# Kernel optimization log

Measured on AMD Instinct MI355X. Metric: run time of the kernel, lower is better.

Reference implementation:

```python
import jax, jax.numpy as jnp
import numpy as np

B, T, EMB_D, HEAD = 8, 2048, 1024, 128


def setup_inputs() -> dict:
    key = jax.random.key(0)
    ks = jax.random.split(key, 7)
    s = 1.0 / np.sqrt(EMB_D)
    return {
        "inputs": jax.random.normal(ks[0], (B, T, EMB_D), dtype=jnp.float32),
        "Wk": jax.random.uniform(ks[1], (EMB_D, HEAD), jnp.float32, -s, s),
        "bk": jax.random.uniform(ks[2], (HEAD,), jnp.float32, -s, s),
        "Wq": jax.random.uniform(ks[3], (EMB_D, HEAD), jnp.float32, -s, s),
        "bq": jax.random.uniform(ks[4], (HEAD,), jnp.float32, -s, s),
        "Wv": jax.random.uniform(ks[5], (EMB_D, HEAD), jnp.float32, -s, s),
        "bv": jax.random.uniform(ks[6], (HEAD,), jnp.float32, -s, s),
    }


def reference(inputs, Wk, bk, Wq, bq, Wv, bv):
    # inputs: [B, T, C]
    Bq, Tq, _ = inputs.shape
    k = inputs @ Wk + bk  # [B, T, H]
    q = inputs @ Wq + bq
    v = inputs @ Wv + bv
    scale = HEAD ** -0.5
    weights = jnp.einsum("bth,bsh->bts", q, k) * scale  # [B, T, T]
    causal = jnp.tril(jnp.ones((Tq, Tq), dtype=bool))
    weights = jnp.where(causal, weights, -jnp.inf)
    # NOTE: original code applies softmax over dim=1 (the query axis), faithfully reproduced
    weights = jax.nn.softmax(weights, axis=1)
    return jnp.einsum("bts,bsh->bth", weights, v)  # [B, T, H]
```

## Files before the change

kernel.cpp:

```cpp
#include <hip/hip_runtime.h>
#include <hip/hip_bf16.h>

#define T_SEQ 2048
#define NBATCH 8
#define EMB 1024
#define HD 128

typedef _Float16 f16_t;
typedef _Float16 f16x8 __attribute__((ext_vector_type(8)));
typedef _Float16 f16x4 __attribute__((ext_vector_type(4)));
typedef float f32x4 __attribute__((ext_vector_type(4)));


__device__ __forceinline__ void g2l(const f16_t* g, f16_t* l) {
    __builtin_amdgcn_global_load_lds(
        (const __attribute__((address_space(1))) unsigned int*)g,
        (__attribute__((address_space(3))) unsigned int*)l, 16, 0, 0);
}

__global__ __launch_bounds__(256) void prep(
    const float* __restrict__ Wk, const float* __restrict__ bk,
    const float* __restrict__ Wq, const float* __restrict__ bq,
    const float* __restrict__ Wv, const float* __restrict__ bv,
    f16_t* __restrict__ w2, float* __restrict__ biasc) {
    int n = blockIdx.x;
    int t = threadIdx.x;
    const float scale = 0.08838834764831845f;
    const float* W; const float* bias; float sc; int col;
    if (n < 128)      { W = Wq; bias = bq; sc = scale; col = n; }
    else if (n < 256) { W = Wk; bias = bk; sc = 1.0f;  col = n - 128; }
    else              { W = Wv; bias = bv; sc = 1.0f;  col = n - 256; }
    if (t < 128) {
        int k0 = t * 8;
        f16x8 v;
        #pragma unroll
        for (int i = 0; i < 8; ++i) v[i] = (f16_t)(W[(size_t)(k0 + i) * HD + col] * sc);
        *(f16x8*)&w2[(size_t)(n >> 4) * 16384 + (size_t)(k0 >> 3) * 128 + (n & 15) * 8] = v;
    }
    if (t == 0) biasc[n] = bias[col] * sc;
}

__global__ __launch_bounds__(256) void qkv_gemm(
    const float* __restrict__ X, const f16_t* __restrict__ w2,
    const float* __restrict__ biasc,
    f16_t* __restrict__ q2, f16_t* __restrict__ k2, f16_t* __restrict__ v2) {
    __shared__ f16_t Xs[2][64 * 72];
    __shared__ __align__(16) f16_t Bl[2][8 * 1024];

    int bid = blockIdx.x;
    int r8 = bid & 7, g = bid >> 3;
    int band = (g / 3) * 8 + r8;
    int i = g % 3;
    int m0 = band * 64, n0 = i * 128;
    int tid = threadIdx.x;
    int lane = tid & 63, w = tid >> 6;
    int quad = lane >> 4, l15 = lane & 15;
    int msub = (w & 1) * 32, nsub = (w >> 1) * 64;

    int srow = tid >> 2;
    int scg  = (tid & 3) * 16;

    const float* xrow = X + (size_t)(m0 + srow) * EMB + scg;
    const f16_t* bbase = w2 + (size_t)(n0 >> 4) * 16384;

    f32x4 acc[2][4] = {};
    float4 pf[4];

    auto loadA = [&](int kc) {
        #pragma unroll
        for (int u = 0; u < 4; ++u) pf[u] = *(const float4*)(xrow + kc * 64 + u * 4);
    };
    auto stageB = [&](int kc, int buf) {
        const f16_t* bsrc = bbase + (size_t)kc * 1024;
        #pragma unroll
        for (int ii = 0; ii < 4; ++ii) {
            int D = tid * 16 + ii * 4096;
            g2l(bsrc + (size_t)(D >> 11) * 16384 + ((D & 2047) >> 1),
                &Bl[buf][D >> 1]);
        }
    };
    auto stageA = [&](int buf) {
        union { f16_t h[8]; uint4 u4; } p0, p1;
        p0.h[0] = (f16_t)pf[0].x; p0.h[1] = (f16_t)pf[0].y;
        p0.h[2] = (f16_t)pf[0].z; p0.h[3] = (f16_t)pf[0].w;
        p0.h[4] = (f16_t)pf[1].x; p0.h[5] = (f16_t)pf[1].y;
        p0.h[6] = (f16_t)pf[1].z; p0.h[7] = (f16_t)pf[1].w;
        p1.h[0] = (f16_t)pf[2].x; p1.h[1] = (f16_t)pf[2].y;
        p1.h[2] = (f16_t)pf[2].z; p1.h[3] = (f16_t)pf[2].w;
        p1.h[4] = (f16_t)pf[3].x; p1.h[5] = (f16_t)pf[3].y;
        p1.h[6] = (f16_t)pf[3].z; p1.h[7] = (f16_t)pf[3].w;
        *(uint4*)&Xs[buf][srow * 72 + scg] = p0.u4;
        *(uint4*)&Xs[buf][srow * 72 + scg + 8] = p1.u4;
    };
    auto compute = [&](int buf) {
        #pragma unroll
        for (int ks = 0; ks < 2; ++ks) {
            f16x8 afr0 = *(const f16x8*)&Xs[buf][(msub + l15) * 72 + ks * 32 + quad * 8];
            f16x8 afr1 = *(const f16x8*)&Xs[buf][(msub + 16 + l15) * 72 + ks * 32 + quad * 8];
            #pragma unroll
            for (int nf = 0; nf < 4; ++nf) {
                int ntl = (nsub >> 4) + nf;
                f16x8 bfr = *(const f16x8*)&Bl[buf][ntl * 1024 + (ks * 4 + quad) * 128 + l15 * 8];
                acc[0][nf] = __builtin_amdgcn_mfma_f32_16x16x32_f16(afr0, bfr, acc[0][nf], 0, 0, 0);
                acc[1][nf] = __builtin_amdgcn_mfma_f32_16x16x32_f16(afr1, bfr, acc[1][nf], 0, 0, 0);
            }
        }
    };

    loadA(0);
    stageB(0, 0);
    stageA(0);
    __syncthreads();

    for (int kc = 0; kc < 16; ++kc) {
        int cur = kc & 1, nxt = cur ^ 1;
        if (kc + 1 < 16) {
            loadA(kc + 1);
            stageB(kc + 1, nxt);
        }
        compute(cur);
        if (kc + 1 < 16) stageA(nxt);
        __syncthreads();
    }

    #pragma unroll
    for (int nf = 0; nf < 4; ++nf) {
        int ng = n0 + nsub + nf * 16 + l15;
        float bval = biasc[ng];
        #pragma unroll
        for (int mf = 0; mf < 2; ++mf) {
            int rowg = m0 + msub + mf * 16 + quad * 4;
            f32x4 a = acc[mf][nf];
            if (ng < 256) {
                f16_t* dst = (ng < 128) ? q2 : k2;
                int c = ng & 127;
                #pragma unroll
                for (int r = 0; r < 4; ++r) {
                    int row = rowg + r;
                    dst[(size_t)(row >> 4) * 2048 + (c >> 3) * 128 + (row & 15) * 8 + (c & 7)]
                        = (f16_t)(a[r] + bval);
                }
            } else {
                int h = ng - 256;
                f16x4 hv;
                #pragma unroll
                for (int r = 0; r < 4; ++r) hv[r] = (f16_t)(a[r] + bval);
                *(f16x4*)&v2[(size_t)(rowg >> 3) * 1024 + h * 8 + (rowg & 7)] = hv;
            }
        }
    }
}

__global__ __launch_bounds__(256, 4) void col_stats(
    const f16_t* __restrict__ q2, const f16_t* __restrict__ k2,
    float* __restrict__ colsum) {
    int bid = blockIdx.x;
    int b = bid & 7;
    int item = 143 - (bid >> 3);
    int cg = 0, slab = 0, cum = 0;
    for (int c = 0; c < 32; ++c) {
        int n = (32 - c + 3) >> 2;
        if (item < cum + n) { cg = c; slab = item - cum; break; }
        cum += n;
    }
    int tc0 = cg + slab * 4, tc1 = min(tc0 + 4, 32);

    int tid = threadIdx.x, lane = tid & 63, w = tid >> 6;
    int quad = lane >> 4, l15 = lane & 15;
    int brow = b * 128;
    size_t base = (size_t)b * T_SEQ;

    f16x8 bfrs[4][4];
    #pragma unroll
    for (int st = 0; st < 4; ++st) {
        const f16_t* kt = k2 + (size_t)(brow + cg * 4 + st) * 2048 + l15 * 8;
        #pragma unroll
        for (int kf = 0; kf < 4; ++kf)
            bfrs[st][kf] = *(const f16x8*)(kt + (kf * 4 + quad) * 128);
    }

    float lacc[4] = {0.f, 0.f, 0.f, 0.f};

    for (int tc = tc0; tc < tc1; ++tc) {
        int tb = tc * 64;
        f16x8 afr[4];
        const f16_t* qt = q2 + (size_t)(brow + tc * 4 + w) * 2048 + l15 * 8;
        #pragma unroll
        for (int kf = 0; kf < 4; ++kf)
            afr[kf] = *(const f16x8*)(qt + (kf * 4 + quad) * 128);
        #pragma unroll
        for (int st = 0; st < 4; ++st) {
            f32x4 s = {};
            #pragma unroll
            for (int kf = 0; kf < 4; ++kf)
                s = __builtin_amdgcn_mfma_f32_16x16x32_f16(afr[kf], bfrs[st][kf], s, 0, 0, 0);
            int scol = cg * 64 + st * 16 + l15;
            #pragma unroll
            for (int r = 0; r < 4; ++r) {
                int t = tb + w * 16 + quad * 4 + r;
                if (t >= scol) lacc[st] += __expf(s[r]);
            }
        }
    }

    #pragma unroll
    for (int st = 0; st < 4; ++st) {
        float v = lacc[st];
        v += __shfl_xor(v, 16, 64);
        v += __shfl_xor(v, 32, 64);
        if (quad == 0) atomicAdd(&colsum[base + cg * 64 + st * 16 + l15], v);
    }
}

__global__ __launch_bounds__(256, 4) void attn_out(
    const f16_t* __restrict__ q2, const f16_t* __restrict__ k2,
    const f16_t* __restrict__ v2, const float* __restrict__ colsum,
    float* __restrict__ out) {
    __shared__ __align__(16) f16_t Kl[4 * 2048];
    __shared__ __align__(16) f16_t Vl[8 * 1024];
    __shared__ __align__(16) f16_t Pl[32 * 72];

    int bid = blockIdx.x;
    int b = bid & 7;
    int item = 159 - (bid >> 3);
    int g = 0, slab = 0, cum = 0;
    for (int gg = 0; gg < 64; ++gg) {
        int n = (((gg >> 1) + 1) + 7) >> 3;
        if (item < cum + n) { g = gg; slab = item - cum; break; }
        cum += n;
    }
    int nch = (g >> 1) + 1;
    int c0 = slab * 8, c1 = min(c0 + 8, nch);
    int trow = g * 32;

    int tid = threadIdx.x, lane = tid & 63, w = tid >> 6;
    int quad = lane >> 4, l15 = lane & 15;
    int brow = b * 128;
    size_t base = (size_t)b * T_SEQ;

    f16x8 qfr[2][4];
    #pragma unroll
    for (int tt = 0; tt < 2; ++tt) {
        const f16_t* qt = q2 + (size_t)(brow + 2 * g + tt) * 2048 + l15 * 8;
        #pragma unroll
        for (int kf = 0; kf < 4; ++kf)
            qfr[tt][kf] = *(const f16x8*)(qt + (kf * 4 + quad) * 128);
    }

    f32x4 o[2][2] = {};

    for (int c = c0; c < c1; ++c) {
        int sb = c * 64;
        __syncthreads();
        const f16_t* ksrc = k2 + (size_t)(brow + (sb >> 4)) * 2048;
        const f16_t* vsrc = v2 + (((size_t)base + sb) >> 3) * 1024;
        #pragma unroll
        for (int i = 0; i < 4; ++i) {
            g2l(ksrc + i * 2048 + tid * 8, Kl + i * 2048 + tid * 8);
            g2l(vsrc + i * 2048 + tid * 8, Vl + i * 2048 + tid * 8);
        }
        __syncthreads();

        float iv = 1.0f / colsum[base + sb + w * 16 + l15];
        int scol = sb + w * 16 + l15;
        f16x8 bfr[4];
        #pragma unroll
        for (int kf = 0; kf < 4; ++kf)
            bfr[kf] = *(const f16x8*)&Kl[w * 2048 + (kf * 4 + quad) * 128 + l15 * 8];
        #pragma unroll
        for (int tt = 0; tt < 2; ++tt) {
            f32x4 s = {};
            #pragma unroll
            for (int kf = 0; kf < 4; ++kf)
                s = __builtin_amdgcn_mfma_f32_16x16x32_f16(qfr[tt][kf], bfr[kf], s, 0, 0, 0);
            #pragma unroll
            for (int r = 0; r < 4; ++r) {
                int t = trow + tt * 16 + quad * 4 + r;
                float pv = (t >= scol) ? __expf(s[r]) * iv : 0.f;
                Pl[(tt * 16 + quad * 4 + r) * 72 + w * 16 + l15] = (f16_t)pv;
            }
        }
        __syncthreads();

        #pragma unroll
        for (int kf2 = 0; kf2 < 2; ++kf2) {
            f16x8 pa0 = *(const f16x8*)&Pl[(l15) * 72 + kf2 * 32 + quad * 8];
            f16x8 pa1 = *(const f16x8*)&Pl[(16 + l15) * 72 + kf2 * 32 + quad * 8];
            #pragma unroll
            for (int hh = 0; hh < 2; ++hh) {
                f16x8 vfr = *(const f16x8*)&Vl[(kf2 * 4 + quad) * 1024 + (w * 32 + hh * 16 + l15) * 8];
                o[0][hh] = __builtin_amdgcn_mfma_f32_16x16x32_f16(pa0, vfr, o[0][hh], 0, 0, 0);
                o[1][hh] = __builtin_amdgcn_mfma_f32_16x16x32_f16(pa1, vfr, o[1][hh], 0, 0, 0);
            }
        }
    }

    #pragma unroll
    for (int tt = 0; tt < 2; ++tt)
        #pragma unroll
        for (int hh = 0; hh < 2; ++hh)
            #pragma unroll
            for (int r = 0; r < 4; ++r)
                atomicAdd(&out[(base + trow + tt * 16 + quad * 4 + r) * HD + w * 32 + hh * 16 + l15],
                          o[tt][hh][r]);
}

extern "C" void kernel_launch(void* const* d_in, const int* in_sizes, int n_in,
                              void* d_out, int out_size, void* d_ws, size_t ws_size,
                              hipStream_t stream) {
    const float* X  = (const float*)d_in[0];
    const float* Wk = (const float*)d_in[1];
    const float* bk = (const float*)d_in[2];
    const float* Wq = (const float*)d_in[3];
    const float* bq = (const float*)d_in[4];
    const float* Wv = (const float*)d_in[5];
    const float* bv = (const float*)d_in[6];
    float* out = (float*)d_out;

    char* ws = (char*)d_ws;
    const size_t W2_B    = 24 * 16384 * 2;
    const size_t BIAS_B  = 2048;
    const size_t QKV_B   = (size_t)NBATCH * T_SEQ * HD * 2;
    f16_t* w2     = (f16_t*)ws;
    float* biasc  = (float*)(ws + W2_B);
    f16_t* q2     = (f16_t*)(ws + W2_B + BIAS_B);
    f16_t* k2     = (f16_t*)(ws + W2_B + BIAS_B + QKV_B);
    f16_t* v2     = (f16_t*)(ws + W2_B + BIAS_B + 2 * QKV_B);
    float* colsum = (float*)(ws + W2_B + BIAS_B + 3 * QKV_B);

    hipMemsetAsync(out, 0, (size_t)NBATCH * T_SEQ * HD * sizeof(float), stream);
    hipMemsetAsync(colsum, 0, (size_t)NBATCH * T_SEQ * sizeof(float), stream);

    prep<<<dim3(384), dim3(256), 0, stream>>>(Wk, bk, Wq, bq, Wv, bv, w2, biasc);
    qkv_gemm<<<dim3(768), dim3(256), 0, stream>>>(X, w2, biasc, q2, k2, v2);
    col_stats<<<dim3(1152), dim3(256), 0, stream>>>(q2, k2, colsum);
    attn_out<<<dim3(1280), dim3(256), 0, stream>>>(q2, k2, v2, colsum, out);
}
```

Measured before the change: 177.6 us.

## Load K/V fragments straight to registers with double-buffered prefetch in attn_out

Drops the shared-memory staging of K and V in attn_out. Each wave now loads its MFMA fragments directly from global memory into registers, prefetching the next chunk while the current one computes, and P is double-buffered in LDS so only one barrier is needed per chunk. This removes LDS traffic and two barriers per chunk, in exchange for higher register pressure (launch bounds lowered from 4 to 3 blocks) and uncoalesced-ish direct global fragment loads.

```diff
diff --git a/kernel.cpp b/kernel.cpp
--- a/kernel.cpp
+++ b/kernel.cpp
@@ -212,13 +212,11 @@
     }
 }
 
-__global__ __launch_bounds__(256, 4) void attn_out(
+__global__ __launch_bounds__(256, 3) void attn_out(
     const f16_t* __restrict__ q2, const f16_t* __restrict__ k2,
     const f16_t* __restrict__ v2, const float* __restrict__ colsum,
     float* __restrict__ out) {
-    __shared__ __align__(16) f16_t Kl[4 * 2048];
-    __shared__ __align__(16) f16_t Vl[8 * 1024];
-    __shared__ __align__(16) f16_t Pl[32 * 72];
+    __shared__ __align__(16) f16_t Pl[2][32 * 72];
 
     int bid = blockIdx.x;
     int b = bid & 7;
@@ -249,50 +247,70 @@
 
     f32x4 o[2][2] = {};
 
-    for (int c = c0; c < c1; ++c) {
-        int sb = c * 64;
-        __syncthreads();
-        const f16_t* ksrc = k2 + (size_t)(brow + (sb >> 4)) * 2048;
-        const f16_t* vsrc = v2 + (((size_t)base + sb) >> 3) * 1024;
-        #pragma unroll
-        for (int i = 0; i < 4; ++i) {
-            g2l(ksrc + i * 2048 + tid * 8, Kl + i * 2048 + tid * 8);
-            g2l(vsrc + i * 2048 + tid * 8, Vl + i * 2048 + tid * 8);
-        }
-        __syncthreads();
-
-        float iv = 1.0f / colsum[base + sb + w * 16 + l15];
-        int scol = sb + w * 16 + l15;
-        f16x8 bfr[4];
+    f16x8 kA[4], kB[4];
+    f16x8 vA[2][2], vB[2][2];
+    float csA, csB;
+
+    auto loadKVc = [&](int c, f16x8 (&k)[4], f16x8 (&v)[2][2], float& cs) {
+        const f16_t* kt = k2 + (size_t)(brow + c * 4 + w) * 2048 + l15 * 8;
         #pragma unroll
         for (int kf = 0; kf < 4; ++kf)
-            bfr[kf] = *(const f16x8*)&Kl[w * 2048 + (kf * 4 + quad) * 128 + l15 * 8];
+            k[kf] = *(const f16x8*)(kt + (kf * 4 + quad) * 128);
+        const f16_t* vt = v2 + ((size_t)(base + c * 64) >> 3) * 1024;
+        #pragma unroll
+        for (int kf2 = 0; kf2 < 2; ++kf2)
+            #pragma unroll
+            for (int hh = 0; hh < 2; ++hh)
+                v[kf2][hh] = *(const f16x8*)&vt[(kf2 * 4 + quad) * 1024 +
+                                                (w * 32 + hh * 16 + l15) * 8];
+        cs = colsum[base + c * 64 + w * 16 + l15];
+    };
+    auto qkt = [&](int c, f16x8 (&k)[4], float cs, int pb) {
+        float iv = 1.0f / cs;
+        int scol = c * 64 + w * 16 + l15;
         #pragma unroll
         for (int tt = 0; tt < 2; ++tt) {
             f32x4 s = {};
             #pragma unroll
             for (int kf = 0; kf < 4; ++kf)
-                s = __builtin_amdgcn_mfma_f32_16x16x32_f16(qfr[tt][kf], bfr[kf], s, 0, 0, 0);
+                s = __builtin_amdgcn_mfma_f32_16x16x32_f16(qfr[tt][kf], k[kf], s, 0, 0, 0);
             #pragma unroll
             for (int r = 0; r < 4; ++r) {
                 int t = trow + tt * 16 + quad * 4 + r;
                 float pv = (t >= scol) ? __expf(s[r]) * iv : 0.f;
-                Pl[(tt * 16 + quad * 4 + r) * 72 + w * 16 + l15] = (f16_t)pv;
-            }
-        }
+                Pl[pb][(tt * 16 + quad * 4 + r) * 72 + w * 16 + l15] = (f16_t)pv;
+            }
+        }
+    };
+    auto pvstep = [&](f16x8 (&v)[2][2], int pb) {
+        #pragma unroll
+        for (int kf2 = 0; kf2 < 2; ++kf2) {
+            f16x8 pa0 = *(const f16x8*)&Pl[pb][(l15) * 72 + kf2 * 32 + quad * 8];
+            f16x8 pa1 = *(const f16x8*)&Pl[pb][(16 + l15) * 72 + kf2 * 32 + quad * 8];
+            #pragma unroll
+            for (int hh = 0; hh < 2; ++hh) {
+                o[0][hh] = __builtin_amdgcn_mfma_f32_16x16x32_f16(pa0, v[kf2][hh], o[0][hh], 0, 0, 0);
+                o[1][hh] = __builtin_amdgcn_mfma_f32_16x16x32_f16(pa1, v[kf2][hh], o[1][hh], 0, 0, 0);
+            }
+        }
+    };
+
+    int c = c0;
+    loadKVc(c, kA, vA, csA);
+    for (; c + 1 < c1; c += 2) {
+        qkt(c, kA, csA, 0);
         __syncthreads();
-
-        #pragma unroll
-        for (int kf2 = 0; kf2 < 2; ++kf2) {
-            f16x8 pa0 = *(const f16x8*)&Pl[(l15) * 72 + kf2 * 32 + quad * 8];
-            f16x8 pa1 = *(const f16x8*)&Pl[(16 + l15) * 72 + kf2 * 32 + quad * 8];
-            #pragma unroll
-            for (int hh = 0; hh < 2; ++hh) {
-                f16x8 vfr = *(const f16x8*)&Vl[(kf2 * 4 + quad) * 1024 + (w * 32 + hh * 16 + l15) * 8];
-                o[0][hh] = __builtin_amdgcn_mfma_f32_16x16x32_f16(pa0, vfr, o[0][hh], 0, 0, 0);
-                o[1][hh] = __builtin_amdgcn_mfma_f32_16x16x32_f16(pa1, vfr, o[1][hh], 0, 0, 0);
-            }
-        }
+        loadKVc(c + 1, kB, vB, csB);
+        pvstep(vA, 0);
+        qkt(c + 1, kB, csB, 1);
+        __syncthreads();
+        if (c + 2 < c1) loadKVc(c + 2, kA, vA, csA);
+        pvstep(vB, 1);
+    }
+    if (c < c1) {
+        qkt(c, kA, csA, 0);
+        __syncthreads();
+        pvstep(vA, 0);
     }
 
     #pragma unroll
```

Result: faster. 174.0 us (-2.0%).

## Materialize exp scores in col_stats and fold column normalization into V

Applied to the files above, without the earlier changes.

col_stats now writes the masked exp(QK^T) tile values as fp16 into a packed lower-triangular workspace while it accumulates column sums. A new v_scale kernel divides each V row by its column sum, so attn_out only streams the stored exp tiles and the scaled V into MFMAs. This removes the second QK^T recomputation, the exp, the LDS staging and the syncthreads from attn_out. In exchange it writes and reads roughly 35 MB of fp16 score data through global memory, adds another launch, and rounds V/colsum to fp16 before the multiply.

```diff
diff --git a/kernel.cpp b/kernel.cpp
--- a/kernel.cpp
+++ b/kernel.cpp
@@ -153,7 +153,7 @@
 
 __global__ __launch_bounds__(256, 4) void col_stats(
     const f16_t* __restrict__ q2, const f16_t* __restrict__ k2,
-    float* __restrict__ colsum) {
+    float* __restrict__ colsum, f16_t* __restrict__ e2) {
     int bid = blockIdx.x;
     int b = bid & 7;
     int item = 143 - (bid >> 3);
@@ -169,6 +169,7 @@
     int quad = lane >> 4, l15 = lane & 15;
     int brow = b * 128;
     size_t base = (size_t)b * T_SEQ;
+    size_t ebb = (size_t)b * 2162688;
 
     f16x8 bfrs[4][4];
     #pragma unroll
@@ -183,6 +184,7 @@
 
     for (int tc = tc0; tc < tc1; ++tc) {
         int tb = tc * 64;
+        size_t ebase = ebb + (size_t)2048 * tc * (tc + 1) + (size_t)w * 1024 * (tc + 1);
         f16x8 afr[4];
         const f16_t* qt = q2 + (size_t)(brow + tc * 4 + w) * 2048 + l15 * 8;
         #pragma unroll
@@ -195,10 +197,15 @@
             for (int kf = 0; kf < 4; ++kf)
                 s = __builtin_amdgcn_mfma_f32_16x16x32_f16(afr[kf], bfrs[st][kf], s, 0, 0, 0);
             int scol = cg * 64 + st * 16 + l15;
+            int s8 = cg * 8 + st * 2 + (l15 >> 3);
+            f16_t* ep = e2 + ebase + (size_t)s8 * 128 + (l15 & 7);
             #pragma unroll
             for (int r = 0; r < 4; ++r) {
                 int t = tb + w * 16 + quad * 4 + r;
-                if (t >= scol) lacc[st] += __expf(s[r]);
+                float e = __expf(s[r]);
+                float ev = (t >= scol) ? e : 0.f;
+                lacc[st] += ev;
+                ep[(quad * 4 + r) * 8] = (f16_t)ev;
             }
         }
     }
@@ -212,14 +219,26 @@
     }
 }
 
+__global__ __launch_bounds__(256) void v_scale(
+    const f16_t* __restrict__ v2, const float* __restrict__ colsum,
+    f16_t* __restrict__ v2s) {
+    int i = blockIdx.x * 256 + threadIdx.x;
+    size_t o = (size_t)i * 8;
+    int rg = (int)(o >> 10);
+    f16x8 v = *(const f16x8*)&v2[o];
+    float4 c0 = *(const float4*)&colsum[rg * 8];
+    float4 c1 = *(const float4*)&colsum[rg * 8 + 4];
+    f16x8 r;
+    r[0] = (f16_t)((float)v[0] / c0.x); r[1] = (f16_t)((float)v[1] / c0.y);
+    r[2] = (f16_t)((float)v[2] / c0.z); r[3] = (f16_t)((float)v[3] / c0.w);
+    r[4] = (f16_t)((float)v[4] / c1.x); r[5] = (f16_t)((float)v[5] / c1.y);
+    r[6] = (f16_t)((float)v[6] / c1.z); r[7] = (f16_t)((float)v[7] / c1.w);
+    *(f16x8*)&v2s[o] = r;
+}
+
 __global__ __launch_bounds__(256, 4) void attn_out(
-    const f16_t* __restrict__ q2, const f16_t* __restrict__ k2,
-    const f16_t* __restrict__ v2, const float* __restrict__ colsum,
+    const f16_t* __restrict__ e2, const f16_t* __restrict__ v2s,
     float* __restrict__ out) {
-    __shared__ __align__(16) f16_t Kl[4 * 2048];
-    __shared__ __align__(16) f16_t Vl[8 * 1024];
-    __shared__ __align__(16) f16_t Pl[32 * 72];
-
     int bid = blockIdx.x;
     int b = bid & 7;
     int item = 159 - (bid >> 3);
@@ -235,64 +254,35 @@
 
     int tid = threadIdx.x, lane = tid & 63, w = tid >> 6;
     int quad = lane >> 4, l15 = lane & 15;
-    int brow = b * 128;
     size_t base = (size_t)b * T_SEQ;
 
-    f16x8 qfr[2][4];
-    #pragma unroll
-    for (int tt = 0; tt < 2; ++tt) {
-        const f16_t* qt = q2 + (size_t)(brow + 2 * g + tt) * 2048 + l15 * 8;
-        #pragma unroll
-        for (int kf = 0; kf < 4; ++kf)
-            qfr[tt][kf] = *(const f16x8*)(qt + (kf * 4 + quad) * 128);
-    }
+    int ct = g >> 1;
+    size_t et1 = (size_t)1024 * (ct + 1);
+    size_t eb = (size_t)b * 2162688 + (size_t)2048 * ct * (ct + 1)
+              + (size_t)((2 * g) & 3) * et1;
 
     f32x4 o[2][2] = {};
 
     for (int c = c0; c < c1; ++c) {
-        int sb = c * 64;
-        __syncthreads();
-        const f16_t* ksrc = k2 + (size_t)(brow + (sb >> 4)) * 2048;
-        const f16_t* vsrc = v2 + (((size_t)base + sb) >> 3) * 1024;
-        #pragma unroll
-        for (int i = 0; i < 4; ++i) {
-            g2l(ksrc + i * 2048 + tid * 8, Kl + i * 2048 + tid * 8);
-            g2l(vsrc + i * 2048 + tid * 8, Vl + i * 2048 + tid * 8);
-        }
-        __syncthreads();
-
-        float iv = 1.0f / colsum[base + sb + w * 16 + l15];
-        int scol = sb + w * 16 + l15;
-        f16x8 bfr[4];
-        #pragma unroll
-        for (int kf = 0; kf < 4; ++kf)
-            bfr[kf] = *(const f16x8*)&Kl[w * 2048 + (kf * 4 + quad) * 128 + l15 * 8];
-        #pragma unroll
-        for (int tt = 0; tt < 2; ++tt) {
-            f32x4 s = {};
-            #pragma unroll
-            for (int kf = 0; kf < 4; ++kf)
-                s = __builtin_amdgcn_mfma_f32_16x16x32_f16(qfr[tt][kf], bfr[kf], s, 0, 0, 0);
-            #pragma unroll
-            for (int r = 0; r < 4; ++r) {
-                int t = trow + tt * 16 + quad * 4 + r;
-                float pv = (t >= scol) ? __expf(s[r]) * iv : 0.f;
-                Pl[(tt * 16 + quad * 4 + r) * 72 + w * 16 + l15] = (f16_t)pv;
+        f16x8 pa[2][2], vf[2][2];
+        const f16_t* vt = v2s + ((size_t)(base + c * 64) >> 3) * 1024;
+        #pragma unroll
+        for (int kf2 = 0; kf2 < 2; ++kf2) {
+            size_t es = eb + (size_t)(c * 8 + kf2 * 4 + quad) * 128 + l15 * 8;
+            pa[0][kf2] = *(const f16x8*)&e2[es];
+            pa[1][kf2] = *(const f16x8*)&e2[es + et1];
+            #pragma unroll
+            for (int hh = 0; hh < 2; ++hh)
+                vf[kf2][hh] = *(const f16x8*)&vt[(kf2 * 4 + quad) * 1024 +
+                                                 (w * 32 + hh * 16 + l15) * 8];
+        }
+        #pragma unroll
+        for (int kf2 = 0; kf2 < 2; ++kf2)
+            #pragma unroll
+            for (int hh = 0; hh < 2; ++hh) {
+                o[0][hh] = __builtin_amdgcn_mfma_f32_16x16x32_f16(pa[0][kf2], vf[kf2][hh], o[0][hh], 0, 0, 0);
+                o[1][hh] = __builtin_amdgcn_mfma_f32_16x16x32_f16(pa[1][kf2], vf[kf2][hh], o[1][hh], 0, 0, 0);
             }
-        }
-        __syncthreads();
-
-        #pragma unroll
-        for (int kf2 = 0; kf2 < 2; ++kf2) {
-            f16x8 pa0 = *(const f16x8*)&Pl[(l15) * 72 + kf2 * 32 + quad * 8];
-            f16x8 pa1 = *(const f16x8*)&Pl[(16 + l15) * 72 + kf2 * 32 + quad * 8];
-            #pragma unroll
-            for (int hh = 0; hh < 2; ++hh) {
-                f16x8 vfr = *(const f16x8*)&Vl[(kf2 * 4 + quad) * 1024 + (w * 32 + hh * 16 + l15) * 8];
-                o[0][hh] = __builtin_amdgcn_mfma_f32_16x16x32_f16(pa0, vfr, o[0][hh], 0, 0, 0);
-                o[1][hh] = __builtin_amdgcn_mfma_f32_16x16x32_f16(pa1, vfr, o[1][hh], 0, 0, 0);
-            }
-        }
     }
 
     #pragma unroll
@@ -321,18 +311,22 @@
     const size_t W2_B    = 24 * 16384 * 2;
     const size_t BIAS_B  = 2048;
     const size_t QKV_B   = (size_t)NBATCH * T_SEQ * HD * 2;
+    const size_t CS_B    = (size_t)NBATCH * T_SEQ * 4;
     f16_t* w2     = (f16_t*)ws;
     float* biasc  = (float*)(ws + W2_B);
     f16_t* q2     = (f16_t*)(ws + W2_B + BIAS_B);
     f16_t* k2     = (f16_t*)(ws + W2_B + BIAS_B + QKV_B);
     f16_t* v2     = (f16_t*)(ws + W2_B + BIAS_B + 2 * QKV_B);
     float* colsum = (float*)(ws + W2_B + BIAS_B + 3 * QKV_B);
+    f16_t* v2s    = (f16_t*)(ws + W2_B + BIAS_B + 3 * QKV_B + CS_B);
+    f16_t* e2     = (f16_t*)(ws + W2_B + BIAS_B + 4 * QKV_B + CS_B);
 
     hipMemsetAsync(out, 0, (size_t)NBATCH * T_SEQ * HD * sizeof(float), stream);
-    hipMemsetAsync(colsum, 0, (size_t)NBATCH * T_SEQ * sizeof(float), stream);
+    hipMemsetAsync(colsum, 0, CS_B, stream);
 
     prep<<<dim3(384), dim3(256), 0, stream>>>(Wk, bk, Wq, bq, Wv, bv, w2, biasc);
     qkv_gemm<<<dim3(768), dim3(256), 0, stream>>>(X, w2, biasc, q2, k2, v2);
-    col_stats<<<dim3(1152), dim3(256), 0, stream>>>(q2, k2, colsum);
-    attn_out<<<dim3(1280), dim3(256), 0, stream>>>(q2, k2, v2, colsum, out);
-}
+    col_stats<<<dim3(1152), dim3(256), 0, stream>>>(q2, k2, colsum, e2);
+    v_scale<<<dim3(1024), dim3(256), 0, stream>>>(v2, colsum, v2s);
+    attn_out<<<dim3(1280), dim3(256), 0, stream>>>(e2, v2s, out);
+}
```

New measurement: 183.7 us. +3.4%, slower.
